# Optimization experiments

Measured on AMD Instinct MI355X. Metric: run time of the kernel, lower is better.

## Reference

```python
import jax, jax.numpy as jnp
import numpy as np

EMBED = 2048
HEADS = 16
HEAD_DIM = EMBED // HEADS
CHUNK = 128
BASE = 10000.0
EPS = 1e-6


def setup_inputs() -> dict:
    key = jax.random.key(0)
    ks = jax.random.split(key, 8)
    b, n, d = 2, 2048, EMBED
    std = 0.02
    return {
        "x": jax.random.normal(ks[0], (b, n, d), jnp.float32),
        "Wq": jax.random.normal(ks[1], (d, d), jnp.float32) * std,
        "Wk": jax.random.normal(ks[2], (d, d), jnp.float32) * std,
        "Wv": jax.random.normal(ks[3], (d, d), jnp.float32) * std,
        "Wo": jax.random.normal(ks[4], (d, d), jnp.float32) * std,
        "Wg1": jax.random.normal(ks[5], (d, HEAD_DIM), jnp.float32) * std,
        "Wg2": jax.random.normal(ks[6], (HEAD_DIM, d), jnp.float32) * std,
        "norm_weight": jnp.ones((d,), jnp.float32),
    }


def _alibi_log_decay(h):
    # lightning attention 'constant' decay: per-head ALiBi slope, log_lambda = -slope
    slopes = 2.0 ** (-8.0 * (jnp.arange(h, dtype=jnp.float32) + 1.0) / h)
    return -slopes  # [h]


def _lrpe_rotate(x):
    # RoPE-like rotation on head_dim (half-split), offset=0
    b, n, h, d = x.shape
    half = d // 2
    theta = BASE ** (-2.0 * jnp.arange(half, dtype=jnp.float32) / d)  # [half]
    ang = jnp.arange(n, dtype=jnp.float32)[:, None] * theta[None, :]  # [n, half]
    cos = jnp.cos(ang)[None, :, None, :]
    sin = jnp.sin(ang)[None, :, None, :]
    x1, x2 = x[..., :half], x[..., half:]
    return jnp.concatenate([x1 * cos - x2 * sin, x1 * sin + x2 * cos], axis=-1)


def _lightning_attn(q, k, v, log_lam):
    # chunk-recurrent linear attention with per-head exponential decay
    b, n, h, d = q.shape
    C = CHUNK
    nc = n // C
    qc = q.reshape(b, nc, C, h, d).transpose(1, 0, 2, 3, 4)  # [nc,b,C,h,d]
    kc = k.reshape(b, nc, C, h, d).transpose(1, 0, 2, 3, 4)
    vc = v.reshape(b, nc, C, h, d).transpose(1, 0, 2, 3, 4)
    i = jnp.arange(C, dtype=jnp.float32)
    diff = i[:, None] - i[None, :]  # [C,C]
    # intra-chunk decay mask D[h,t,s] = lambda_h^(t-s) for t>=s else 0
    D = jnp.where(diff[None] >= 0, jnp.exp(log_lam[:, None, None] * diff[None]), 0.0)
    decay_q = jnp.exp(log_lam[None, :] * (i[:, None] + 1.0))    # [C,h]
    decay_k = jnp.exp(log_lam[None, :] * (C - 1.0 - i[:, None]))  # [C,h]
    lam_C = jnp.exp(log_lam * C)  # [h]

    def step(S, qkv):
        qi, ki, vi = qkv  # [b,C,h,d]
        scores = jnp.einsum('bthd,bshd->bhts', qi, ki) * D[None]
        o_intra = jnp.einsum('bhts,bshd->bthd', scores, vi)
        o_inter = jnp.einsum('bthd,bhde->bthe', qi * decay_q[None, :, :, None], S)
        S_new = lam_C[None, :, None, None] * S + jnp.einsum(
            'bshd,bshe->bhde', ki * decay_k[None, :, :, None], vi)
        return S_new, o_intra + o_inter

    S0 = jnp.zeros((b, h, d, d), q.dtype)
    _, o = jax.lax.scan(step, S0, (qc, kc, vc))  # o: [nc,b,C,h,d]
    return o.transpose(1, 0, 2, 3, 4).reshape(b, n, h, d)


def _gated_group_rmsnorm(o, gate, weight):
    # gate_pos='pre', gate_act='sigmoid', num_groups=HEADS
    b, n, d = o.shape
    x = o * jax.nn.sigmoid(gate)
    xg = x.reshape(b, n, HEADS, HEAD_DIM)
    ms = jnp.mean(xg * xg, axis=-1, keepdims=True)
    xg = xg * jax.lax.rsqrt(ms + EPS)
    return xg.reshape(b, n, d) * weight


def reference(x, Wq, Wk, Wv, Wo, Wg1, Wg2, norm_weight):
    b, n, d = x.shape
    q = (x @ Wq).reshape(b, n, HEADS, HEAD_DIM)
    k = (x @ Wk).reshape(b, n, HEADS, HEAD_DIM)
    v = (x @ Wv).reshape(b, n, HEADS, HEAD_DIM)
    q = jax.nn.silu(q)
    k = jax.nn.silu(k)
    q = _lrpe_rotate(q)
    k = _lrpe_rotate(k)
    log_lam = _alibi_log_decay(HEADS)
    o = _lightning_attn(q, k, v, log_lam).reshape(b, n, d)
    gate = (x @ Wg1) @ Wg2
    o = _gated_group_rmsnorm(o, gate, norm_weight)
    return o @ Wo
```

## Files before the change

### kernel.cpp

```cpp
#include <hip/hip_runtime.h>


#define DEV __device__ __forceinline__
typedef unsigned short u16;
typedef __bf16 bf16x8 __attribute__((ext_vector_type(8)));
typedef float f32x4 __attribute__((ext_vector_type(4)));
typedef u16 u16x8 __attribute__((ext_vector_type(8)));
typedef u16 u16x4 __attribute__((ext_vector_type(4)));

DEV u16 f2bf(float f) {
  unsigned u = __builtin_bit_cast(unsigned, f);
  u += 0x7fffu + ((u >> 16) & 1u);
  return (u16)(u >> 16);
}
DEV float bf2f(u16 h) {
  unsigned u = ((unsigned)h) << 16;
  return __builtin_bit_cast(float, u);
}
DEV void async16(const u16* g, u16* l) {
  __builtin_amdgcn_global_load_lds(
      (const __attribute__((address_space(1))) unsigned int*)g,
      (__attribute__((address_space(3))) unsigned int*)l, 16, 0, 0);
}

__global__ void prep_all(const float* __restrict__ x,
                         const float* __restrict__ Wq, const float* __restrict__ Wk,
                         const float* __restrict__ Wv, const float* __restrict__ Wo,
                         const float* __restrict__ Wg1, const float* __restrict__ Wg2,
                         u16* __restrict__ xb, u16* __restrict__ wtqkvg,
                         u16* __restrict__ wot, u16* __restrict__ wg2t,
                         float* __restrict__ rope) {
  int id = blockIdx.x;
  if (id < 8192) {
    long i = ((long)id * 256 + threadIdx.x) * 4;
    float4 v = *(const float4*)(x + i);
    ushort4 p;
    p.x = f2bf(v.x); p.y = f2bf(v.y); p.z = f2bf(v.z); p.w = f2bf(v.w);
    *(ushort4*)(xb + i) = p;
    return;
  }
  if (id >= 25088) {
    int idx = (id - 25088) * 256 + threadIdx.x;
    int t = idx >> 6, jj = idx & 63;
    float th = exp2f(-13.287712379549449f * (float)jj * (1.f / 64.f));
    float sn, cs;
    sincosf((float)t * th, &sn, &cs);
    ((float2*)rope)[idx] = make_float2(cs, sn);
    return;
  }
  id -= 8192;
  __shared__ float t[32][33];
  const float* in; u16* out; int K, N, bx, by;
  bool perm = false;
  if (id < 12288) {
    int w = id >> 12, tt = id & 4095;
    in = (w == 0) ? Wq : (w == 1) ? Wk : Wv;
    out = wtqkvg + (long)w * 2048 * 2048;
    K = 2048; N = 2048; bx = tt & 63; by = tt >> 6;
    perm = (w < 2);
  } else if (id < 16384) {
    int tt = id - 12288;
    in = Wo; out = wot; K = 2048; N = 2048; bx = tt & 63; by = tt >> 6;
  } else if (id < 16640) {
    int tt = id - 16384;
    in = Wg1; out = wtqkvg + 6144L * 2048; K = 2048; N = 128; bx = tt & 3; by = tt >> 2;
  } else {
    int tt = id - 16640;
    in = Wg2; out = wg2t; K = 128; N = 2048; bx = tt & 63; by = tt >> 6;
  }
  int c = threadIdx.x & 31, r0 = threadIdx.x >> 5;
  for (int r = r0; r < 32; r += 8)
    t[r][c] = in[(long)(by * 32 + r) * N + bx * 32 + c];
  __syncthreads();
  for (int r = r0; r < 32; r += 8) {
    int n = bx * 32 + r, nr = n;
    if (perm) {
      int h = n >> 7, j = n & 127, jj = j & 63, hi = j >> 6;
      nr = h * 128 + (jj & 15) + 32 * (jj >> 4) + 16 * hi;
    }
    out[(long)nr * K + by * 32 + c] = f2bf(t[c][r]);
  }
}

template <typename OutT>
__global__ __launch_bounds__(256, 4) void gemm_bt(
    const u16* __restrict__ A, const u16* __restrict__ B, OutT* __restrict__ C,
    int M, int N, int K, int lda, int ldb, int ldc, int rot,
    int nc, long sA1, long sA2, long sB1, long sB2, long sC1, long sC2,
    const float* __restrict__ rope, u16* __restrict__ VT) {
  __shared__ u16 smem[8192];
  u16* const sA = smem;
  u16* const sB = smem + 4096;
  {
    int z = blockIdx.z, z1 = z / nc, z2 = z % nc;
    A += z1 * sA1 + z2 * sA2;
    B += z1 * sB1 + z2 * sB2;
    C += z1 * sC1 + z2 * sC2;
  }
  int bxs, bys;
  {
    int lin = blockIdx.x + gridDim.x * blockIdx.y;
    int per = 16 * gridDim.y;
    int g = lin / per, r = lin % per;
    int base = g * 16;
    int w = min(16, (int)gridDim.x - base);
    bxs = base + r % w; bys = r / w;
  }
  const int tid = threadIdx.x, lane = tid & 63, wid = tid >> 6;
  const int bm = bys * 128, bn = bxs * 128;
  const int ch0 = wid * 2, ch1 = ch0 + 1;
  const int lr = lane >> 2;
  const int ak = (((lane & 3) - ((lane >> 3) & 3)) & 3) * 8;
  const int ar0 = ch0 * 16 + lr, ar1 = ch1 * 16 + lr;
  const u16* gA0 = A + (long)(bm + ar0) * lda + ak;
  const u16* gA1 = A + (long)(bm + ar1) * lda + ak;
  const u16* gB0 = B + (long)(bn + ar0) * ldb + ak;
  const u16* gB1 = B + (long)(bn + ar1) * ldb + ak;
  u16* lA0 = sA + ch0 * 512; u16* lA1 = sA + ch1 * 512;
  u16* lB0 = sB + ch0 * 512; u16* lB1 = sB + ch1 * 512;
  const int wm = (wid & 1) * 64, wn = (wid >> 1) * 64;
  const int fm = lane & 15, kq = lane >> 4;
  const int qs = ((kq + (fm >> 1)) & 3) * 8;
  const int aoff = (wm >> 4) * 512 + fm * 32 + qs;
  const int boff = (wn >> 4) * 512 + fm * 32 + qs;
  f32x4 acc[4][4] = {};
  for (int kb = 0; kb < K; kb += 32) {
    async16(gA0, lA0); async16(gA1, lA1);
    async16(gB0, lB0); async16(gB1, lB1);
    gA0 += 32; gA1 += 32; gB0 += 32; gB1 += 32;
    __syncthreads();
    bf16x8 af[4], bfr[4];
#pragma unroll
    for (int i = 0; i < 4; i++) af[i] = *(const bf16x8*)&sA[aoff + i * 512];
#pragma unroll
    for (int i = 0; i < 4; i++) bfr[i] = *(const bf16x8*)&sB[boff + i * 512];
#pragma unroll
    for (int mt = 0; mt < 4; mt++)
#pragma unroll
      for (int nt = 0; nt < 4; nt++)
        acc[mt][nt] = __builtin_amdgcn_mfma_f32_16x16x32_bf16(af[mt], bfr[nt], acc[mt][nt], 0, 0, 0);
    __syncthreads();
  }
  const int cr = (lane >> 4) * 4;
  if constexpr (sizeof(OutT) == 2) {
    if (rot == 1 && bn < 4096) {
#pragma unroll
      for (int mt = 0; mt < 4; mt++)
#pragma unroll
        for (int r = 0; r < 4; r++) {
          long row = bm + wm + mt * 16 + cr + r;
          const float2* rp = (const float2*)rope + (long)(row & 2047) * 64;
#pragma unroll
          for (int np = 0; np < 4; np += 2) {
            float x1 = acc[mt][np][r], x2 = acc[mt][np + 1][r];
            x1 = x1 / (1.f + __expf(-x1));
            x2 = x2 / (1.f + __expf(-x2));
            int jj = fm + 16 * ((wn >> 5) + (np >> 1));
            float2 cn = rp[jj];
            C[row * ldc + bn + jj]      = f2bf(x1 * cn.x - x2 * cn.y);
            C[row * ldc + bn + 64 + jj] = f2bf(x1 * cn.y + x2 * cn.x);
          }
        }
      return;
    }
    if (rot == 1 && bn < 6144) {
      const int bq = bm >> 11;
      const int head = (bn - 4096) >> 7;
      const int tb = bm & 2047;
      u16* vbase = VT + (long)(bq * 16 + head) * 128 * 2048 + tb;
      u16* const sV = smem;
#pragma unroll
      for (int dh = 0; dh < 2; dh++) {
        __syncthreads();
        if ((wid >> 1) == dh) {
#pragma unroll
          for (int mt = 0; mt < 4; mt++)
#pragma unroll
            for (int nt = 0; nt < 4; nt++) {
              int dl = nt * 16 + fm;
              int t0 = wm + mt * 16 + cr;
              u16x4 pk;
#pragma unroll
              for (int r = 0; r < 4; r++) pk[r] = f2bf(acc[mt][nt][r]);
              *(u16x4*)&sV[dl * 128 + (t0 ^ ((fm & 15) << 3))] = pk;
            }
        }
        __syncthreads();
#pragma unroll
        for (int it = 0; it < 4; it++) {
          int dl = it * 16 + (tid >> 4);
          int tc = (tid & 15) * 8;
          u16x8 vv = *(const u16x8*)&sV[dl * 128 + (tc ^ ((dl & 15) << 3))];
          *(u16x8*)(vbase + (long)(dh * 64 + dl) * 2048 + tc) = vv;
        }
      }
      return;
    }
  }
#pragma unroll
  for (int mt = 0; mt < 4; mt++)
#pragma unroll
    for (int nt = 0; nt < 4; nt++)
#pragma unroll
      for (int r = 0; r < 4; r++) {
        long row = bm + wm + mt * 16 + cr + r;
        long col = bn + wn + nt * 16 + fm;
        float v = acc[mt][nt][r];
        if constexpr (sizeof(OutT) == 2) {
          if (rot == 2) v = 1.f / (1.f + __expf(-v));
          C[row * ldc + col] = f2bf(v);
        } else {
          C[row * ldc + col] = v;
        }
      }
}

__global__ void transpose_k(const u16* __restrict__ qkv, u16* __restrict__ kdT) {
  __shared__ float t[32][33];
  int bh = blockIdx.z;
  int b = bh >> 4, h = bh & 15;
  int n0 = blockIdx.x * 32, d0 = blockIdx.y * 32;
  int cc = threadIdx.x & 31, rr0 = threadIdx.x >> 5;
  float log_lam = -exp2f(-0.5f * (float)(h + 1));
  for (int rr = rr0; rr < 32; rr += 8) {
    int n = n0 + rr;
    float v = bf2f(qkv[(long)(b * 2048 + n) * 6272 + 2048 + h * 128 + d0 + cc]);
    v *= expf(log_lam * (float)(127 - (n & 127)));
    t[rr][cc] = v;
  }
  __syncthreads();
  for (int rr = rr0; rr < 32; rr += 8)
    kdT[((long)bh * 128 + d0 + rr) * 2048 + n0 + cc] = f2bf(t[cc][rr]);
}

__global__ void scan_state(const u16* __restrict__ U, u16* __restrict__ S_all) {
  int blk = blockIdx.x;
  int bh = blk >> 3, sl = blk & 7, h = bh & 15;
  float log_lam = -exp2f(-0.5f * (float)(h + 1));
  float lamC = expf(log_lam * 128.f);
  long off = (long)bh * 16 * 16384 + sl * 2048 + threadIdx.x * 8;
  float s[8];
#pragma unroll
  for (int j = 0; j < 8; j++) s[j] = 0.f;
  for (int c = 0; c < 16; c++) {
    long idx = off + (long)c * 16384;
    u16x8 sb;
#pragma unroll
    for (int j = 0; j < 8; j++) sb[j] = f2bf(s[j]);
    *(u16x8*)(S_all + idx) = sb;
    u16x8 ub = *(const u16x8*)(U + idx);
#pragma unroll
    for (int j = 0; j < 8; j++) s[j] = lamC * s[j] + bf2f(ub[j]);
  }
}

__global__ __launch_bounds__(256, 2) void attn_out(
    const u16* __restrict__ qkv, const u16* __restrict__ vT,
    const u16* __restrict__ S_all, const u16* __restrict__ gate,
    const float* __restrict__ nw, u16* __restrict__ nrm) {
  __shared__ u16 sA[128 * 32], sB[128 * 32], sK[128 * 32];
  __shared__ u16 sS[128 * 136];
  __shared__ float sNorm[2][128];
  const int blk = blockIdx.x;
  const int bh = blk >> 4, c = blk & 15;
  const int b = bh >> 4, h = bh & 15;
  const float log_lam = -exp2f(-0.5f * (float)(h + 1));
  const int tid = threadIdx.x, lane = tid & 63, wid = tid >> 6;
  const int wm = (wid & 1) * 64, wn = (wid >> 1) * 64;
  const int fm = lane & 15, fq = lane >> 4, kq = lane >> 4;
  const int lr = lane >> 2;
  const int ak = (((lane & 3) - ((lane >> 3) & 3)) & 3) * 8;
  const int ch0 = wid * 2, ch1 = ch0 + 1;
  const int r0 = ch0 * 16 + lr, r1 = ch1 * 16 + lr;
  const int qs = ((kq + (fm >> 1)) & 3) * 8;
  const int aoff = (wm >> 4) * 512 + fm * 32 + qs;
  const int boff = (wn >> 4) * 512 + fm * 32 + qs;
  const u16* qbase = qkv + (long)(b * 2048 + c * 128) * 6272 + h * 128;
  const u16* kbase = qbase + 2048;
  const u16* Sbase = S_all + ((long)bh * 16 + c) * 16384;
  const u16* vbase = vT + (long)bh * 262144 + (long)c * 128;

  f32x4 acc[4][4] = {};
  f32x4 sc[4][4] = {};
  for (int kb = 0; kb < 128; kb += 32) {
    async16(qbase + (long)r0 * 6272 + kb + ak, sA + ch0 * 512);
    async16(qbase + (long)r1 * 6272 + kb + ak, sA + ch1 * 512);
    async16(Sbase + r0 * 128 + kb + ak, sB + ch0 * 512);
    async16(Sbase + r1 * 128 + kb + ak, sB + ch1 * 512);
    async16(kbase + (long)r0 * 6272 + kb + ak, sK + ch0 * 512);
    async16(kbase + (long)r1 * 6272 + kb + ak, sK + ch1 * 512);
    __syncthreads();
    bf16x8 aq[4], bs[4], bk[4];
#pragma unroll
    for (int i = 0; i < 4; i++) {
      aq[i] = *(const bf16x8*)&sA[aoff + i * 512];
      bs[i] = *(const bf16x8*)&sB[boff + i * 512];
      bk[i] = *(const bf16x8*)&sK[boff + i * 512];
    }
#pragma unroll
    for (int mt = 0; mt < 4; mt++)
#pragma unroll
      for (int nt = 0; nt < 4; nt++) {
        acc[mt][nt] = __builtin_amdgcn_mfma_f32_16x16x32_bf16(aq[mt], bs[nt], acc[mt][nt], 0, 0, 0);
        sc[mt][nt] = __builtin_amdgcn_mfma_f32_16x16x32_bf16(aq[mt], bk[nt], sc[mt][nt], 0, 0, 0);
      }
    __syncthreads();
  }
#pragma unroll
  for (int mt = 0; mt < 4; mt++)
#pragma unroll
    for (int r = 0; r < 4; r++) {
      int t = wm + mt * 16 + fq * 4 + r;
      float d = __expf(log_lam * (float)(t + 1));
#pragma unroll
      for (int nt = 0; nt < 4; nt++) acc[mt][nt][r] *= d;
    }
  float eS[4];
#pragma unroll
  for (int nt = 0; nt < 4; nt++)
    eS[nt] = __expf(log_lam * (float)(63 - (nt * 16 + fm)));
#pragma unroll
  for (int mt = 0; mt < 4; mt++)
#pragma unroll
    for (int r = 0; r < 4; r++) {
      int t = wm + mt * 16 + fq * 4 + r;
      float eT = __expf(log_lam * (float)(t - wn - 63));
#pragma unroll
      for (int nt = 0; nt < 4; nt++) {
        int s = wn + nt * 16 + fm;
        float v = sc[mt][nt][r];
        v = (t >= s) ? v * (eT * eS[nt]) : 0.f;
        sS[t * 136 + s] = f2bf(v);
      }
    }
  __syncthreads();
  for (int kb = 0; kb < 128; kb += 32) {
    async16(vbase + r0 * 2048 + kb + ak, sB + ch0 * 512);
    async16(vbase + r1 * 2048 + kb + ak, sB + ch1 * 512);
    __syncthreads();
    bf16x8 as[4], bv[4];
#pragma unroll
    for (int i = 0; i < 4; i++) {
      as[i] = *(const bf16x8*)&sS[(wm + i * 16 + fm) * 136 + kb + kq * 8];
      bv[i] = *(const bf16x8*)&sB[boff + i * 512];
    }
#pragma unroll
    for (int mt = 0; mt < 4; mt++)
#pragma unroll
      for (int nt = 0; nt < 4; nt++)
        acc[mt][nt] = __builtin_amdgcn_mfma_f32_16x16x32_bf16(as[mt], bv[nt], acc[mt][nt], 0, 0, 0);
    __syncthreads();
  }
  const u16* gbase = gate + (long)(b * 2048 + c * 128) * 2048 + h * 128;
  float nwv[4];
#pragma unroll
  for (int nt = 0; nt < 4; nt++) nwv[nt] = nw[h * 128 + wn + nt * 16 + fm];
  float part[4][4];
#pragma unroll
  for (int mt = 0; mt < 4; mt++)
#pragma unroll
    for (int r = 0; r < 4; r++) {
      int t = wm + mt * 16 + fq * 4 + r;
      float p = 0.f;
#pragma unroll
      for (int nt = 0; nt < 4; nt++) {
        int e = wn + nt * 16 + fm;
        float g = bf2f(gbase[(long)t * 2048 + e]);
        float x = acc[mt][nt][r] * g;
        acc[mt][nt][r] = x;
        p += x * x;
      }
      part[mt][r] = p;
    }
#pragma unroll
  for (int o = 1; o < 16; o <<= 1)
#pragma unroll
    for (int mt = 0; mt < 4; mt++)
#pragma unroll
      for (int r = 0; r < 4; r++) part[mt][r] += __shfl_xor(part[mt][r], o);
  if (fm == 0) {
#pragma unroll
    for (int mt = 0; mt < 4; mt++)
#pragma unroll
      for (int r = 0; r < 4; r++)
        sNorm[wid >> 1][wm + mt * 16 + fq * 4 + r] = part[mt][r];
  }
  __syncthreads();
  long orow0 = (long)(b * 2048 + c * 128);
#pragma unroll
  for (int mt = 0; mt < 4; mt++)
#pragma unroll
    for (int r = 0; r < 4; r++) {
      int t = wm + mt * 16 + fq * 4 + r;
      float ms = (sNorm[0][t] + sNorm[1][t]) * (1.f / 128.f);
      float rs = rsqrtf(ms + 1e-6f);
#pragma unroll
      for (int nt = 0; nt < 4; nt++) {
        int e = wn + nt * 16 + fm;
        nrm[(orow0 + t) * 2048 + h * 128 + e] = f2bf(acc[mt][nt][r] * rs * nwv[nt]);
      }
    }
}

extern "C" void kernel_launch(void* const* d_in, const int* in_sizes, int n_in,
                              void* d_out, int out_size, void* d_ws, size_t ws_size,
                              hipStream_t stream) {
  (void)in_sizes; (void)n_in; (void)out_size; (void)ws_size;
  const float* x   = (const float*)d_in[0];
  const float* Wq  = (const float*)d_in[1];
  const float* Wk  = (const float*)d_in[2];
  const float* Wv  = (const float*)d_in[3];
  const float* Wo  = (const float*)d_in[4];
  const float* Wg1 = (const float*)d_in[5];
  const float* Wg2 = (const float*)d_in[6];
  const float* nw  = (const float*)d_in[7];
  float* out = (float*)d_out;

  char* ws = (char*)d_ws;
  size_t off = 0;
  auto alloc = [&](size_t bytes) -> void* {
    void* p = ws + off;
    off += (bytes + 255) & ~(size_t)255;
    return p;
  };
  u16* xb    = (u16*)alloc(4096UL * 2048 * 2);
  u16* wtqkv = (u16*)alloc(6272UL * 2048 * 2);
  u16* wot   = (u16*)alloc(2048UL * 2048 * 2);
  u16* wg2t  = (u16*)alloc(2048UL * 128 * 2);
  u16* qkvg  = (u16*)alloc(4096UL * 6272 * 2);
  u16* gate  = (u16*)alloc(4096UL * 2048 * 2);
  u16* kdT   = (u16*)alloc(32UL * 128 * 2048 * 2);
  u16* vT    = (u16*)alloc(32UL * 128 * 2048 * 2);
  u16* Ubuf  = (u16*)alloc(512UL * 16384 * 2);
  u16* S_all = (u16*)alloc(512UL * 16384 * 2);
  u16* nrm   = (u16*)alloc(4096UL * 2048 * 2);
  float* rope = (float*)alloc(2048UL * 64 * 8);

  prep_all<<<dim3(25600), dim3(256), 0, stream>>>(x, Wq, Wk, Wv, Wo, Wg1, Wg2,
                                                  xb, wtqkv, wot, wg2t, rope);
  gemm_bt<u16><<<dim3(49, 32, 1), dim3(256), 0, stream>>>(xb, wtqkv, qkvg,
      4096, 6272, 2048, 2048, 2048, 6272, 1, 1, 0, 0, 0, 0, 0, 0, rope, vT);
  gemm_bt<u16><<<dim3(16, 32, 1), dim3(256), 0, stream>>>(qkvg + 6144, wg2t, gate,
      4096, 2048, 128, 6272, 128, 2048, 2, 1, 0, 0, 0, 0, 0, 0, nullptr, nullptr);
  transpose_k<<<dim3(64, 4, 32), dim3(256), 0, stream>>>(qkvg, kdT);
  gemm_bt<u16><<<dim3(1, 1, 512), dim3(256), 0, stream>>>(vT, kdT, Ubuf,
      128, 128, 128, 2048, 2048, 128, 0,
      16, 262144L, 128L, 262144L, 128L, 262144L, 16384L, nullptr, nullptr);
  scan_state<<<dim3(256), dim3(256), 0, stream>>>(Ubuf, S_all);
  attn_out<<<dim3(512), dim3(256), 0, stream>>>(qkvg, vT, S_all, gate, nw, nrm);
  gemm_bt<float><<<dim3(16, 32, 1), dim3(256), 0, stream>>>(nrm, wot, out,
      4096, 2048, 2048, 2048, 2048, 2048, 0, 1, 0, 0, 0, 0, 0, 0, nullptr, nullptr);
}
```

Before: 398.6 us.

## Fuse decayed K transpose into QKV GEMM epilogue and gate GEMM into attn_out

The QKV GEMM epilogue now also writes a decay-scaled, transposed copy of rotated K into kdT through shared memory, which removes the separate transpose_k kernel. The gate projection (g1 @ Wg2) is recomputed per tile inside attn_out with MFMA, and its sigmoid is applied in registers. This drops the standalone gate GEMM kernel and the full 4096x2048 bf16 gate buffer round trip. In exchange the QKV epilogue does extra syncs and transcendental work, and attn_out runs one more small K=128 MFMA loop.

```diff
diff --git a/kernel.cpp b/kernel.cpp
--- a/kernel.cpp
+++ b/kernel.cpp
@@ -87,7 +87,7 @@
     const u16* __restrict__ A, const u16* __restrict__ B, OutT* __restrict__ C,
     int M, int N, int K, int lda, int ldb, int ldc, int rot,
     int nc, long sA1, long sA2, long sB1, long sB2, long sC1, long sC2,
-    const float* __restrict__ rope, u16* __restrict__ VT) {
+    const float* __restrict__ rope, u16* __restrict__ VT, u16* __restrict__ KT) {
   __shared__ u16 smem[8192];
   u16* const sA = smem;
   u16* const sB = smem + 4096;
@@ -161,6 +161,50 @@
             C[row * ldc + bn + 64 + jj] = f2bf(x1 * cn.y + x2 * cn.x);
           }
         }
+      if (bn >= 2048) {
+        const int head = (bn - 2048) >> 7;
+        const int bq = bm >> 11, tb = bm & 2047;
+        const float llk = -exp2f(-0.5f * (float)(head + 1));
+        const float em = __expf(-llk);
+        u16* kt = KT + (long)(bq * 16 + head) * 128 * 2048 + tb;
+        u16* const sV = smem;
+#pragma unroll
+        for (int half = 0; half < 2; half++) {
+          __syncthreads();
+#pragma unroll
+          for (int mt = 0; mt < 4; mt++) {
+            int t0 = wm + mt * 16 + cr;
+            float d0 = __expf(llk * (float)(127 - t0));
+#pragma unroll
+            for (int np = 0; np < 4; np += 2) {
+              int jj = fm + 16 * ((wn >> 5) + (np >> 1));
+              u16x4 pk;
+              float dd = d0;
+#pragma unroll
+              for (int r = 0; r < 4; r++) {
+                long row = bm + t0 + r;
+                float2 cn = ((const float2*)rope)[(long)(row & 2047) * 64 + jj];
+                float x1 = acc[mt][np][r], x2 = acc[mt][np + 1][r];
+                x1 = x1 / (1.f + __expf(-x1));
+                x2 = x2 / (1.f + __expf(-x2));
+                float y = (half == 0) ? (x1 * cn.x - x2 * cn.y)
+                                      : (x1 * cn.y + x2 * cn.x);
+                pk[r] = f2bf(y * dd);
+                dd *= em;
+              }
+              *(u16x4*)&sV[jj * 128 + (t0 ^ ((jj & 15) << 3))] = pk;
+            }
+          }
+          __syncthreads();
+#pragma unroll
+          for (int it = 0; it < 4; it++) {
+            int dl = it * 16 + (tid >> 4);
+            int tc = (tid & 15) * 8;
+            u16x8 vv = *(const u16x8*)&sV[dl * 128 + (tc ^ ((dl & 15) << 3))];
+            *(u16x8*)(kt + (long)(half * 64 + dl) * 2048 + tc) = vv;
+          }
+        }
+      }
       return;
     }
     if (rot == 1 && bn < 6144) {
@@ -206,31 +250,9 @@
         long row = bm + wm + mt * 16 + cr + r;
         long col = bn + wn + nt * 16 + fm;
         float v = acc[mt][nt][r];
-        if constexpr (sizeof(OutT) == 2) {
-          if (rot == 2) v = 1.f / (1.f + __expf(-v));
-          C[row * ldc + col] = f2bf(v);
-        } else {
-          C[row * ldc + col] = v;
-        }
-      }
-}
-
-__global__ void transpose_k(const u16* __restrict__ qkv, u16* __restrict__ kdT) {
-  __shared__ float t[32][33];
-  int bh = blockIdx.z;
-  int b = bh >> 4, h = bh & 15;
-  int n0 = blockIdx.x * 32, d0 = blockIdx.y * 32;
-  int cc = threadIdx.x & 31, rr0 = threadIdx.x >> 5;
-  float log_lam = -exp2f(-0.5f * (float)(h + 1));
-  for (int rr = rr0; rr < 32; rr += 8) {
-    int n = n0 + rr;
-    float v = bf2f(qkv[(long)(b * 2048 + n) * 6272 + 2048 + h * 128 + d0 + cc]);
-    v *= expf(log_lam * (float)(127 - (n & 127)));
-    t[rr][cc] = v;
-  }
-  __syncthreads();
-  for (int rr = rr0; rr < 32; rr += 8)
-    kdT[((long)bh * 128 + d0 + rr) * 2048 + n0 + cc] = f2bf(t[cc][rr]);
+        if constexpr (sizeof(OutT) == 2) C[row * ldc + col] = f2bf(v);
+        else                             C[row * ldc + col] = v;
+      }
 }
 
 __global__ void scan_state(const u16* __restrict__ U, u16* __restrict__ S_all) {
@@ -256,7 +278,7 @@
 
 __global__ __launch_bounds__(256, 2) void attn_out(
     const u16* __restrict__ qkv, const u16* __restrict__ vT,
-    const u16* __restrict__ S_all, const u16* __restrict__ gate,
+    const u16* __restrict__ S_all, const u16* __restrict__ wg2t,
     const float* __restrict__ nw, u16* __restrict__ nrm) {
   __shared__ u16 sA[128 * 32], sB[128 * 32], sK[128 * 32];
   __shared__ u16 sS[128 * 136];
@@ -277,8 +299,10 @@
   const int boff = (wn >> 4) * 512 + fm * 32 + qs;
   const u16* qbase = qkv + (long)(b * 2048 + c * 128) * 6272 + h * 128;
   const u16* kbase = qbase + 2048;
+  const u16* g1base = qkv + (long)(b * 2048 + c * 128) * 6272 + 6144;
   const u16* Sbase = S_all + ((long)bh * 16 + c) * 16384;
   const u16* vbase = vT + (long)bh * 262144 + (long)c * 128;
+  const u16* wbase = wg2t + (long)(h * 128) * 128;
 
   f32x4 acc[4][4] = {};
   f32x4 sc[4][4] = {};
@@ -351,7 +375,26 @@
         acc[mt][nt] = __builtin_amdgcn_mfma_f32_16x16x32_bf16(as[mt], bv[nt], acc[mt][nt], 0, 0, 0);
     __syncthreads();
   }
-  const u16* gbase = gate + (long)(b * 2048 + c * 128) * 2048 + h * 128;
+  f32x4 gsc[4][4] = {};
+  for (int kb = 0; kb < 128; kb += 32) {
+    async16(g1base + (long)r0 * 6272 + kb + ak, sA + ch0 * 512);
+    async16(g1base + (long)r1 * 6272 + kb + ak, sA + ch1 * 512);
+    async16(wbase + r0 * 128 + kb + ak, sB + ch0 * 512);
+    async16(wbase + r1 * 128 + kb + ak, sB + ch1 * 512);
+    __syncthreads();
+    bf16x8 ag[4], bw[4];
+#pragma unroll
+    for (int i = 0; i < 4; i++) {
+      ag[i] = *(const bf16x8*)&sA[aoff + i * 512];
+      bw[i] = *(const bf16x8*)&sB[boff + i * 512];
+    }
+#pragma unroll
+    for (int mt = 0; mt < 4; mt++)
+#pragma unroll
+      for (int nt = 0; nt < 4; nt++)
+        gsc[mt][nt] = __builtin_amdgcn_mfma_f32_16x16x32_bf16(ag[mt], bw[nt], gsc[mt][nt], 0, 0, 0);
+    __syncthreads();
+  }
   float nwv[4];
 #pragma unroll
   for (int nt = 0; nt < 4; nt++) nwv[nt] = nw[h * 128 + wn + nt * 16 + fm];
@@ -360,12 +403,10 @@
   for (int mt = 0; mt < 4; mt++)
 #pragma unroll
     for (int r = 0; r < 4; r++) {
-      int t = wm + mt * 16 + fq * 4 + r;
       float p = 0.f;
 #pragma unroll
       for (int nt = 0; nt < 4; nt++) {
-        int e = wn + nt * 16 + fm;
-        float g = bf2f(gbase[(long)t * 2048 + e]);
+        float g = 1.f / (1.f + __expf(-gsc[mt][nt][r]));
         float x = acc[mt][nt][r] * g;
         acc[mt][nt][r] = x;
         p += x * x;
@@ -428,7 +469,6 @@
   u16* wot   = (u16*)alloc(2048UL * 2048 * 2);
   u16* wg2t  = (u16*)alloc(2048UL * 128 * 2);
   u16* qkvg  = (u16*)alloc(4096UL * 6272 * 2);
-  u16* gate  = (u16*)alloc(4096UL * 2048 * 2);
   u16* kdT   = (u16*)alloc(32UL * 128 * 2048 * 2);
   u16* vT    = (u16*)alloc(32UL * 128 * 2048 * 2);
   u16* Ubuf  = (u16*)alloc(512UL * 16384 * 2);
@@ -439,15 +479,12 @@
   prep_all<<<dim3(25600), dim3(256), 0, stream>>>(x, Wq, Wk, Wv, Wo, Wg1, Wg2,
                                                   xb, wtqkv, wot, wg2t, rope);
   gemm_bt<u16><<<dim3(49, 32, 1), dim3(256), 0, stream>>>(xb, wtqkv, qkvg,
-      4096, 6272, 2048, 2048, 2048, 6272, 1, 1, 0, 0, 0, 0, 0, 0, rope, vT);
-  gemm_bt<u16><<<dim3(16, 32, 1), dim3(256), 0, stream>>>(qkvg + 6144, wg2t, gate,
-      4096, 2048, 128, 6272, 128, 2048, 2, 1, 0, 0, 0, 0, 0, 0, nullptr, nullptr);
-  transpose_k<<<dim3(64, 4, 32), dim3(256), 0, stream>>>(qkvg, kdT);
+      4096, 6272, 2048, 2048, 2048, 6272, 1, 1, 0, 0, 0, 0, 0, 0, rope, vT, kdT);
   gemm_bt<u16><<<dim3(1, 1, 512), dim3(256), 0, stream>>>(vT, kdT, Ubuf,
       128, 128, 128, 2048, 2048, 128, 0,
-      16, 262144L, 128L, 262144L, 128L, 262144L, 16384L, nullptr, nullptr);
+      16, 262144L, 128L, 262144L, 128L, 262144L, 16384L, nullptr, nullptr, nullptr);
   scan_state<<<dim3(256), dim3(256), 0, stream>>>(Ubuf, S_all);
-  attn_out<<<dim3(512), dim3(256), 0, stream>>>(qkvg, vT, S_all, gate, nw, nrm);
+  attn_out<<<dim3(512), dim3(256), 0, stream>>>(qkvg, vT, S_all, wg2t, nw, nrm);
   gemm_bt<float><<<dim3(16, 32, 1), dim3(256), 0, stream>>>(nrm, wot, out,
-      4096, 2048, 2048, 2048, 2048, 2048, 0, 1, 0, 0, 0, 0, 0, 0, nullptr, nullptr);
-}
+      4096, 2048, 2048, 2048, 2048, 2048, 0, 1, 0, 0, 0, 0, 0, 0, nullptr, nullptr, nullptr);
+}
```

Result: faster. 380.1 us (-4.6%).
